# Performance work log

Hardware: AMD Instinct MI355X
Metric: run time of the kernel (lower is better)

The kernel has to match this reference:

```python
import jax, jax.numpy as jnp
import numpy as np

DECAY_CONSTANT = 1.0


def _build_decay_matrices(weight, decay_value, S, dtype):
    """Build the row-repeat and col-repeat upper-triangular decay matrices.

    Wr[i, j] = w0[i] * (clip(dv0,0.9,1) ** (j-i) / C)   for j >= i, else 0
    Wc[i, j] = w1[j] *  clip(dv1,0.9,1) ** ((j-i) / C)  for j >= i, else 0
    """
    i = jnp.arange(S)[:, None]
    j = jnp.arange(S)[None, :]
    mask = j >= i
    # Clamp exponent to 0 in the masked-out (lower-triangular) region so the
    # power never overflows; values there are discarded by the mask anyway.
    e = jnp.where(mask, (j - i).astype(dtype), jnp.asarray(0.0, dtype))
    dv0 = jnp.clip(decay_value[0, 0], 0.9, 1.0).astype(dtype)
    dv1 = jnp.clip(decay_value[1, 0], 0.9, 1.0).astype(dtype)
    w0 = weight[0].astype(dtype)
    w1 = weight[1].astype(dtype)
    Wr = jnp.where(mask, w0[:, None] * ((dv0 ** e) / DECAY_CONSTANT), jnp.asarray(0.0, dtype))
    Wc = jnp.where(mask, w1[None, :] * (dv1 ** (e / DECAY_CONSTANT)), jnp.asarray(0.0, dtype))
    return Wr, Wc


def setup_inputs() -> dict:
    key = jax.random.key(0)
    kx, kw = jax.random.split(key)
    B, E, S = 4, 2048, 2048
    x = jax.random.normal(kx, (B, E, S), dtype=jnp.float32)
    weight = jax.random.normal(kw, (2, S), dtype=jnp.float32)
    bias = jnp.zeros((S,), dtype=jnp.float32)
    decay_value = jnp.ones((2, 1), dtype=jnp.float32)
    return {"x": x, "weight": weight, "bias": bias, "decay_value": decay_value}


def reference(x, weight, bias, decay_value):
    B, E, S = x.shape
    Wr, Wc = _build_decay_matrices(weight, decay_value, S, x.dtype)
    # x @ Wr + x @ Wc == x @ (Wr + Wc); contract the S axis.
    out = jnp.einsum('bes,st->bet', x, Wr + Wc)  # [B, E, S]
    out = out + bias.astype(x.dtype)
    return out
```

## Files before the change

### kernel.cpp

```cpp
#include <hip/hip_runtime.h>


#define S_LEN 2048
#define THREADS 256
#define RPB 4

typedef float f4 __attribute__((ext_vector_type(4)));

__global__ __launch_bounds__(THREADS, 4)
void crcl_kernel(const float* __restrict__ x,
                 const float* __restrict__ weight,
                 const float* __restrict__ bias,
                 const float* __restrict__ decay,
                 float* __restrict__ out,
                 int nrows)
{
    __shared__ float carry[2][RPB][4];

    const int t    = (int)threadIdx.x;
    const int lane = t & 63;
    const int w    = t >> 6;
    const long row0 = (long)blockIdx.x * RPB;

    const f4* w04 = (const f4*)weight;
    const f4* w14 = (const f4*)(weight + S_LEN);
    const f4* b4  = (const f4*)bias;
    const f4 wa = w04[2 * t], wb = w04[2 * t + 1];
    const f4 va = w14[2 * t], vb = w14[2 * t + 1];
    const f4 ba = b4[2 * t],  bb = b4[2 * t + 1];

    f4 xa[RPB], xb[RPB];
#pragma unroll
    for (int r = 0; r < RPB; ++r) {
        long rr = row0 + r; if (rr >= nrows) rr = nrows - 1;
        const f4* x4 = (const f4*)(x + rr * (long)S_LEN);
        xa[r] = x4[2 * t];
        xb[r] = x4[2 * t + 1];
    }

    const float dv0 = fminf(fmaxf(decay[0], 0.9f), 1.0f);
    const float dv1 = fminf(fmaxf(decay[1], 0.9f), 1.0f);

    float pc[RPB], qc[RPB];
#pragma unroll
    for (int r = 0; r < RPB; ++r) {
        float pcr = 0.0f, qcr = 0.0f;
#pragma unroll
        for (int j = 0; j < 4; ++j) {
            pcr = fmaf(dv0, pcr, xa[r][j] * wa[j]);
            qcr = fmaf(dv1, qcr, xa[r][j]);
        }
#pragma unroll
        for (int j = 0; j < 4; ++j) {
            pcr = fmaf(dv0, pcr, xb[r][j] * wb[j]);
            qcr = fmaf(dv1, qcr, xb[r][j]);
        }
        pc[r] = pcr; qc[r] = qcr;
    }

    float A8_0 = dv0 * dv0; A8_0 *= A8_0; A8_0 *= A8_0;
    float A8_1 = dv1 * dv1; A8_1 *= A8_1; A8_1 *= A8_1;

    float cp[RPB], cq[RPB];
#pragma unroll
    for (int r = 0; r < RPB; ++r) { cp[r] = pc[r]; cq[r] = qc[r]; }

    float k0 = A8_0, k1 = A8_1;
#pragma unroll
    for (int d = 1; d < 64; d <<= 1) {
#pragma unroll
        for (int r = 0; r < RPB; ++r) {
            const float up = __shfl_up(cp[r], (unsigned)d, 64);
            const float uq = __shfl_up(cq[r], (unsigned)d, 64);
            if (lane >= d) {
                cp[r] = fmaf(k0, up, cp[r]);
                cq[r] = fmaf(k1, uq, cq[r]);
            }
        }
        k0 *= k0;
        k1 *= k1;
    }

    float cin_p[RPB], cin_q[RPB];
#pragma unroll
    for (int r = 0; r < RPB; ++r) {
        cin_p[r] = __shfl_up(cp[r], 1u, 64);
        cin_q[r] = __shfl_up(cq[r], 1u, 64);
        if (lane == 0) { cin_p[r] = 0.0f; cin_q[r] = 0.0f; }
    }

    if (lane == 63) {
#pragma unroll
        for (int r = 0; r < RPB; ++r) {
            carry[0][r][w] = cp[r];
            carry[1][r][w] = cq[r];
        }
    }
    __syncthreads();

    float A512_0 = A8_0, A512_1 = A8_1;
#pragma unroll
    for (int b = 0; b < 6; ++b) { A512_0 *= A512_0; A512_1 *= A512_1; }

    const float e8 = (float)(8 * lane);
    const float pwl_0 = exp2f(e8 * log2f(dv0));
    const float pwl_1 = exp2f(e8 * log2f(dv1));

#pragma unroll
    for (int r = 0; r < RPB; ++r) {
        float cwp = 0.0f, cwq = 0.0f;
#pragma unroll
        for (int v = 0; v < 3; ++v) {
            if (v < w) {
                cwp = fmaf(cwp, A512_0, carry[0][r][v]);
                cwq = fmaf(cwq, A512_1, carry[1][r][v]);
            }
        }
        cin_p[r] = fmaf(cwp, pwl_0, cin_p[r]);
        cin_q[r] = fmaf(cwq, pwl_1, cin_q[r]);
    }

#pragma unroll
    for (int r = 0; r < RPB; ++r) {
        long rr = row0 + r; if (rr >= nrows) rr = nrows - 1;
        float p2 = cin_p[r], q2 = cin_q[r];
        f4 ya, yb;
#pragma unroll
        for (int j = 0; j < 4; ++j) {
            p2 = fmaf(dv0, p2, xa[r][j] * wa[j]);
            q2 = fmaf(dv1, q2, xa[r][j]);
            ya[j] = fmaf(va[j], q2, p2) + ba[j];
        }
#pragma unroll
        for (int j = 0; j < 4; ++j) {
            p2 = fmaf(dv0, p2, xb[r][j] * wb[j]);
            q2 = fmaf(dv1, q2, xb[r][j]);
            yb[j] = fmaf(vb[j], q2, p2) + bb[j];
        }
        f4* o4 = (f4*)(out + rr * (long)S_LEN);
        __builtin_nontemporal_store(ya, &o4[2 * t]);
        __builtin_nontemporal_store(yb, &o4[2 * t + 1]);
    }
}

extern "C" void kernel_launch(void* const* d_in, const int* in_sizes, int n_in,
                              void* d_out, int out_size, void* d_ws, size_t ws_size,
                              hipStream_t stream) {
    const float* x      = (const float*)d_in[0];
    const float* weight = (const float*)d_in[1];
    const float* bias   = (const float*)d_in[2];
    const float* decay  = (const float*)d_in[3];
    float* out = (float*)d_out;

    const int nrows   = in_sizes[0] / S_LEN;
    const int nblocks = (nrows + RPB - 1) / RPB;
    hipLaunchKernelGGL(crcl_kernel, dim3(nblocks), dim3(THREADS), 0, stream,
                       x, weight, bias, decay, out, nrows);
}
```

Baseline: 29.17 us.

## Process rows one at a time with double-buffered x prefetch and per-row barriers

Restructures the kernel so that each of the block's four rows is handled in sequence: the scan, carry exchange and output write for one row run while the next row's x values are prefetched into a second register buffer. This cuts register pressure from holding all rows at once and overlaps global loads with the shuffle scan, aiming for better latency hiding or occupancy. In exchange it adds four block barriers (raw s_barrier with manual waitcnt and sched_barrier) instead of one, which serialises the warps more often per block.

```diff
diff --git a/kernel.cpp b/kernel.cpp
--- a/kernel.cpp
+++ b/kernel.cpp
@@ -15,7 +15,7 @@
                  float* __restrict__ out,
                  int nrows)
 {
-    __shared__ float carry[2][RPB][4];
+    __shared__ float carry[RPB][2][4];
 
     const int t    = (int)threadIdx.x;
     const int lane = t & 63;
@@ -29,115 +29,98 @@
     const f4 va = w14[2 * t], vb = w14[2 * t + 1];
     const f4 ba = b4[2 * t],  bb = b4[2 * t + 1];
 
-    f4 xa[RPB], xb[RPB];
-#pragma unroll
-    for (int r = 0; r < RPB; ++r) {
-        long rr = row0 + r; if (rr >= nrows) rr = nrows - 1;
-        const f4* x4 = (const f4*)(x + rr * (long)S_LEN);
-        xa[r] = x4[2 * t];
-        xb[r] = x4[2 * t + 1];
-    }
-
     const float dv0 = fminf(fmaxf(decay[0], 0.9f), 1.0f);
     const float dv1 = fminf(fmaxf(decay[1], 0.9f), 1.0f);
 
-    float pc[RPB], qc[RPB];
-#pragma unroll
-    for (int r = 0; r < RPB; ++r) {
-        float pcr = 0.0f, qcr = 0.0f;
-#pragma unroll
-        for (int j = 0; j < 4; ++j) {
-            pcr = fmaf(dv0, pcr, xa[r][j] * wa[j]);
-            qcr = fmaf(dv1, qcr, xa[r][j]);
-        }
-#pragma unroll
-        for (int j = 0; j < 4; ++j) {
-            pcr = fmaf(dv0, pcr, xb[r][j] * wb[j]);
-            qcr = fmaf(dv1, qcr, xb[r][j]);
-        }
-        pc[r] = pcr; qc[r] = qcr;
-    }
-
     float A8_0 = dv0 * dv0; A8_0 *= A8_0; A8_0 *= A8_0;
     float A8_1 = dv1 * dv1; A8_1 *= A8_1; A8_1 *= A8_1;
-
-    float cp[RPB], cq[RPB];
-#pragma unroll
-    for (int r = 0; r < RPB; ++r) { cp[r] = pc[r]; cq[r] = qc[r]; }
-
-    float k0 = A8_0, k1 = A8_1;
-#pragma unroll
-    for (int d = 1; d < 64; d <<= 1) {
-#pragma unroll
-        for (int r = 0; r < RPB; ++r) {
-            const float up = __shfl_up(cp[r], (unsigned)d, 64);
-            const float uq = __shfl_up(cq[r], (unsigned)d, 64);
-            if (lane >= d) {
-                cp[r] = fmaf(k0, up, cp[r]);
-                cq[r] = fmaf(k1, uq, cq[r]);
-            }
-        }
-        k0 *= k0;
-        k1 *= k1;
-    }
-
-    float cin_p[RPB], cin_q[RPB];
-#pragma unroll
-    for (int r = 0; r < RPB; ++r) {
-        cin_p[r] = __shfl_up(cp[r], 1u, 64);
-        cin_q[r] = __shfl_up(cq[r], 1u, 64);
-        if (lane == 0) { cin_p[r] = 0.0f; cin_q[r] = 0.0f; }
-    }
-
-    if (lane == 63) {
-#pragma unroll
-        for (int r = 0; r < RPB; ++r) {
-            carry[0][r][w] = cp[r];
-            carry[1][r][w] = cq[r];
-        }
-    }
-    __syncthreads();
-
     float A512_0 = A8_0, A512_1 = A8_1;
 #pragma unroll
     for (int b = 0; b < 6; ++b) { A512_0 *= A512_0; A512_1 *= A512_1; }
-
     const float e8 = (float)(8 * lane);
     const float pwl_0 = exp2f(e8 * log2f(dv0));
     const float pwl_1 = exp2f(e8 * log2f(dv1));
 
+    f4 x0a, x0b, x1a, x1b;
+    {
+        long rr = row0; if (rr >= nrows) rr = nrows - 1;
+        const f4* p = (const f4*)(x + rr * (long)S_LEN);
+        x0a = p[2 * t]; x0b = p[2 * t + 1];
+    }
+
 #pragma unroll
     for (int r = 0; r < RPB; ++r) {
+        if (r + 1 < RPB) {
+            long rn = row0 + r + 1; if (rn >= nrows) rn = nrows - 1;
+            const f4* p = (const f4*)(x + rn * (long)S_LEN);
+            if ((r & 1) == 0) { x1a = p[2 * t]; x1b = p[2 * t + 1]; }
+            else              { x0a = p[2 * t]; x0b = p[2 * t + 1]; }
+        }
+        const f4 xA = (r & 1) ? x1a : x0a;
+        const f4 xB = (r & 1) ? x1b : x0b;
+
+        float pc = 0.0f, qc = 0.0f;
+#pragma unroll
+        for (int j = 0; j < 4; ++j) {
+            pc = fmaf(dv0, pc, xA[j] * wa[j]);
+            qc = fmaf(dv1, qc, xA[j]);
+        }
+#pragma unroll
+        for (int j = 0; j < 4; ++j) {
+            pc = fmaf(dv0, pc, xB[j] * wb[j]);
+            qc = fmaf(dv1, qc, xB[j]);
+        }
+
+        float cp = pc, cq = qc, k0 = A8_0, k1 = A8_1;
+#pragma unroll
+        for (int d = 1; d < 64; d <<= 1) {
+            const float up = __shfl_up(cp, (unsigned)d, 64);
+            const float uq = __shfl_up(cq, (unsigned)d, 64);
+            if (lane >= d) {
+                cp = fmaf(k0, up, cp);
+                cq = fmaf(k1, uq, cq);
+            }
+            k0 *= k0;
+            k1 *= k1;
+        }
+        float cin_p = __shfl_up(cp, 1u, 64);
+        float cin_q = __shfl_up(cq, 1u, 64);
+        if (lane == 0) { cin_p = 0.0f; cin_q = 0.0f; }
+
+        if (lane == 63) { carry[r][0][w] = cp; carry[r][1][w] = cq; }
+        asm volatile("s_waitcnt lgkmcnt(0)" ::: "memory");
+        __builtin_amdgcn_sched_barrier(0);
+        __builtin_amdgcn_s_barrier();
+        __builtin_amdgcn_sched_barrier(0);
+
         float cwp = 0.0f, cwq = 0.0f;
 #pragma unroll
         for (int v = 0; v < 3; ++v) {
             if (v < w) {
-                cwp = fmaf(cwp, A512_0, carry[0][r][v]);
-                cwq = fmaf(cwq, A512_1, carry[1][r][v]);
+                cwp = fmaf(cwp, A512_0, carry[r][0][v]);
+                cwq = fmaf(cwq, A512_1, carry[r][1][v]);
             }
         }
-        cin_p[r] = fmaf(cwp, pwl_0, cin_p[r]);
-        cin_q[r] = fmaf(cwq, pwl_1, cin_q[r]);
-    }
+        cin_p = fmaf(cwp, pwl_0, cin_p);
+        cin_q = fmaf(cwq, pwl_1, cin_q);
 
-#pragma unroll
-    for (int r = 0; r < RPB; ++r) {
-        long rr = row0 + r; if (rr >= nrows) rr = nrows - 1;
-        float p2 = cin_p[r], q2 = cin_q[r];
+        float p2 = cin_p, q2 = cin_q;
         f4 ya, yb;
 #pragma unroll
         for (int j = 0; j < 4; ++j) {
-            p2 = fmaf(dv0, p2, xa[r][j] * wa[j]);
-            q2 = fmaf(dv1, q2, xa[r][j]);
+            p2 = fmaf(dv0, p2, xA[j] * wa[j]);
+            q2 = fmaf(dv1, q2, xA[j]);
             ya[j] = fmaf(va[j], q2, p2) + ba[j];
         }
 #pragma unroll
         for (int j = 0; j < 4; ++j) {
-            p2 = fmaf(dv0, p2, xb[r][j] * wb[j]);
-            q2 = fmaf(dv1, q2, xb[r][j]);
+            p2 = fmaf(dv0, p2, xB[j] * wb[j]);
+            q2 = fmaf(dv1, q2, xB[j]);
             yb[j] = fmaf(vb[j], q2, p2) + bb[j];
         }
-        f4* o4 = (f4*)(out + rr * (long)S_LEN);
+
+        long rs = row0 + r; if (rs >= nrows) rs = nrows - 1;
+        f4* o4 = (f4*)(out + rs * (long)S_LEN);
         __builtin_nontemporal_store(ya, &o4[2 * t]);
         __builtin_nontemporal_store(yb, &o4[2 * t + 1]);
     }
```

After: 32.00 us. 1.1x slower.
